# Performance work log

Measured on AMD Instinct MI355X. Metric: run time of the kernel, lower is better.

Reference implementation:

```python
import jax, jax.numpy as jnp
import numpy as np
import math

B, S, H = 2, 4096, 512
NUM_HEADS = 8
HEAD_DIM = H // NUM_HEADS
RECENCY_DECAY = 0.9


def setup_inputs() -> dict:
    key = jax.random.key(0)
    k1, k2, k3 = jax.random.split(key, 3)
    scale = 1.0 / math.sqrt(H)
    x = jax.random.normal(k1, (B, S, H), dtype=jnp.float32)
    w_qkv = jax.random.normal(k2, (3 * H, H), dtype=jnp.float32) * scale
    w_out = jax.random.normal(k3, (H, H), dtype=jnp.float32) * scale
    b_out = jnp.zeros((H,), dtype=jnp.float32)
    return {"x": x, "w_qkv": w_qkv, "w_out": w_out, "b_out": b_out}


def reference(x, w_qkv, w_out, b_out):
    batch, seq_len, hidden = x.shape
    nh, hd = NUM_HEADS, HEAD_DIM
    # qkv projection (no bias): torch Linear computes x @ W.T
    qkv = jnp.einsum('bsh,oh->bso', x, w_qkv)
    qkv = qkv.reshape(batch, seq_len, 3, nh, hd)
    q, k, v = jnp.transpose(qkv, (2, 0, 3, 1, 4))  # each [B, nh, S, hd]
    attn = jnp.einsum('bhqd,bhkd->bhqk', q, k) / math.sqrt(hd)
    # recency bias: positions[i, j] = j - i; bias = (j-i)*log(decay) for j<=i else 0
    pos = jnp.arange(seq_len)[None, :] - jnp.arange(seq_len)[:, None]
    bias = jnp.where(pos <= 0, pos.astype(jnp.float32) * math.log(RECENCY_DECAY),
                     jnp.zeros((), dtype=jnp.float32))
    attn = jax.nn.softmax(attn + bias[None, None, :, :], axis=-1)
    out = jnp.einsum('bhqk,bhkd->bqhd', attn, v).reshape(batch, seq_len, hidden)
    return jnp.einsum('bsh,oh->bso', out, w_out) + b_out
```

## Files before the change

kernel.cpp:

```cpp
#include <hip/hip_runtime.h>
#include <hip/hip_bf16.h>
#include <stdint.h>

#define B_   2
#define S_   4096
#define H_   512
#define NH_  8
#define HD_  64
#define M_   (B_*S_)
#define LOG2D (-0.15200309344504997f)
#define SC2   (0.18033688011112042f)

#define NFULL        6
#define NCHUNK       8

typedef __attribute__((ext_vector_type(8))) short bf16x8_t;
typedef __attribute__((ext_vector_type(4))) float f32x4_t;

__device__ __forceinline__ void gl_lds16(const __hip_bfloat16* g, __hip_bfloat16* l) {
  __builtin_amdgcn_global_load_lds(
      (__attribute__((address_space(1))) void*)(g),
      (__attribute__((address_space(3))) void*)(l),
      16, 0, 0);
}

__global__ __launch_bounds__(256)
void cast3_kernel(const float* __restrict__ x, const float* __restrict__ wq,
                  const float* __restrict__ wo,
                  __hip_bfloat16* __restrict__ xb, __hip_bfloat16* __restrict__ wqb,
                  __hip_bfloat16* __restrict__ wob) {
  const int N0 = M_ * H_;
  const int N1 = 3 * H_ * H_;
  int i4 = (blockIdx.x * blockDim.x + threadIdx.x) * 4;
  const float* src; __hip_bfloat16* dst; int off;
  if (i4 < N0)           { src = x;  dst = xb;  off = i4; }
  else if (i4 < N0 + N1) { src = wq; dst = wqb; off = i4 - N0; }
  else                   { src = wo; dst = wob; off = i4 - N0 - N1; }
  float4 v = *(const float4*)(src + off);
  ushort4 o;
  __hip_bfloat16 h;
  h = __float2bfloat16(v.x); o.x = *(unsigned short*)&h;
  h = __float2bfloat16(v.y); o.y = *(unsigned short*)&h;
  h = __float2bfloat16(v.z); o.z = *(unsigned short*)&h;
  h = __float2bfloat16(v.w); o.w = *(unsigned short*)&h;
  *(ushort4*)((unsigned short*)dst + off) = o;
}

template<int EPI>
__global__ __launch_bounds__(256)
void gemm_bt(const __hip_bfloat16* __restrict__ A,
             const __hip_bfloat16* __restrict__ Bw,
             int K,
             __hip_bfloat16* __restrict__ qb,
             __hip_bfloat16* __restrict__ kb,
             __hip_bfloat16* __restrict__ vtb,
             float* __restrict__ outp,
             const float* __restrict__ bias) {
  __shared__ alignas(16) __hip_bfloat16 sA[128*32];
  __shared__ alignas(16) __hip_bfloat16 sB[128*32];
  const int tid  = threadIdx.x;
  const int wave = tid >> 6, lane = tid & 63;
  const int quad = lane >> 4, l15 = lane & 15;
  const int wr = (wave >> 1) * 64, wc = (wave & 1) * 64;
  const int m0 = blockIdx.y * 128, n0 = blockIdx.x * 128;

  f32x4_t acc[4][4] = {};

  for (int kt = 0; kt < K; kt += 32) {
    __syncthreads();
    #pragma unroll
    for (int cc = 0; cc < 2; cc++) {
      int c   = wave * 2 + cc;
      int row = c * 16 + (lane >> 2);
      int col = (lane & 3) * 8;
      gl_lds16(A  + (size_t)(m0 + row) * K + kt + col, sA + c * 512);
      gl_lds16(Bw + (size_t)(n0 + row) * K + kt + col, sB + c * 512);
    }
    __syncthreads();
    bf16x8_t af[4], bfr[4];
    #pragma unroll
    for (int x = 0; x < 4; x++)
      af[x] = *(const bf16x8_t*)(sA + (wr + x*16 + l15)*32 + quad*8);
    #pragma unroll
    for (int y = 0; y < 4; y++)
      bfr[y] = *(const bf16x8_t*)(sB + (wc + y*16 + l15)*32 + quad*8);
    #pragma unroll
    for (int x = 0; x < 4; x++)
      #pragma unroll
      for (int y = 0; y < 4; y++)
        acc[x][y] = __builtin_amdgcn_mfma_f32_16x16x32_bf16(af[x], bfr[y], acc[x][y], 0, 0, 0);
  }

  #pragma unroll
  for (int x = 0; x < 4; x++) {
    #pragma unroll
    for (int y = 0; y < 4; y++) {
      #pragma unroll
      for (int r = 0; r < 4; r++) {
        int gr = m0 + wr + x*16 + quad*4 + r;
        int gc = n0 + wc + y*16 + l15;
        float v = acc[x][y][r];
        if (EPI == 0) {
          int bb = gr >> 12, s = gr & 4095;
          int t  = gc >> 9,  rem = gc & 511;
          int h  = rem >> 6, d = rem & 63;
          __hip_bfloat16 hv = __float2bfloat16(v);
          int bh = bb * NH_ + h;
          if (t == 0)      qb [((size_t)bh * S_ + s) * HD_ + d] = hv;
          else if (t == 1) kb [((size_t)bh * S_ + s) * HD_ + d] = hv;
          else             vtb[((size_t)bh * HD_ + d) * S_ + s] = hv;
        } else {
          outp[(size_t)gr * H_ + gc] = v + bias[gc];
        }
      }
    }
  }
}

__device__ __forceinline__ void stage_kv(const __hip_bfloat16* __restrict__ kb,
                                         const __hip_bfloat16* __restrict__ vtb,
                                         int bh, int j0,
                                         __hip_bfloat16* dK, __hip_bfloat16* dV,
                                         int wave, int lane) {
  const int subK  = lane >> 3;
  const int plogK = (lane & 7) ^ subK;
  const int subV  = lane >> 4;
  #pragma unroll
  for (int cc = 0; cc < 4; cc++) {
    int c = wave * 4 + cc;
    int rK = c * 8 + subK;
    gl_lds16(kb + ((size_t)bh * S_ + j0 + rK) * HD_ + plogK * 8, dK + c * 512);
    int rV = c * 4 + subV;
    int plogV = (lane & 15) ^ (rV & 15);
    gl_lds16(vtb + ((size_t)bh * HD_ + rV) * S_ + j0 + plogV * 8, dV + c * 512);
  }
}

__global__ __launch_bounds__(256)
void attn_kernel(const __hip_bfloat16* __restrict__ qb,
                 const __hip_bfloat16* __restrict__ kb,
                 const __hip_bfloat16* __restrict__ vtb,
                 __hip_bfloat16* __restrict__ ob,
                 float* __restrict__ pO,
                 float* __restrict__ pl) {
  __shared__ alignas(16) __hip_bfloat16 sK[2][128*64];
  __shared__ alignas(16) __hip_bfloat16 sV[2][64*128];
  __shared__ alignas(16) __hip_bfloat16 sP[4][16*128];

  const int tid  = threadIdx.x;
  const int wave = tid >> 6, lane = tid & 63;
  const int quad = lane >> 4, l15 = lane & 15;
  const int w  = blockIdx.x;
  const int bh = blockIdx.y;

  int qt, jt0;
  bool direct;
  if (w < 58) { qt = 6 + w;     jt0 = 0;            direct = true;  }
  else        { int t = w - 58; qt = t >> 3; jt0 = (t & 7) * 4; direct = false; }
  const int q0 = qt * 64;

  const int qr = q0 + wave * 16 + l15;
  const __hip_bfloat16* qrow = qb + ((size_t)bh * S_ + qr) * HD_;
  bf16x8_t aQ0 = *(const bf16x8_t*)(qrow + quad * 8);
  bf16x8_t aQ1 = *(const bf16x8_t*)(qrow + 32 + quad * 8);

  f32x4_t accO[4] = {};
  float l_r[4];
  float negM2[4];
  const int row_i = q0 + wave * 16 + quad * 4;
  #pragma unroll
  for (int r = 0; r < 4; r++) {
    l_r[r] = 0.f;
    negM2[r] = -(17.312340f - LOG2D * (float)(row_i + r));
  }

  stage_kv(kb, vtb, bh, jt0 * 128, &sK[0][0], &sV[0][0], wave, lane);

  for (int it = 0; it < 4; ++it) {
    const int j0 = (jt0 + it) * 128;
    __syncthreads();
    if (it < 3)
      stage_kv(kb, vtb, bh, (jt0 + it + 1) * 128,
               &sK[(it + 1) & 1][0], &sV[(it + 1) & 1][0], wave, lane);

    const __hip_bfloat16* cK = &sK[it & 1][0];
    const __hip_bfloat16* cV = &sV[it & 1][0];

    f32x4_t sfr[8];
    #pragma unroll
    for (int ni = 0; ni < 8; ni++) {
      int row = ni * 16 + l15;
      f32x4_t a = {};
      bf16x8_t b0 = *(const bf16x8_t*)(cK + row * 64 + ((quad       ^ (row & 7)) << 3));
      bf16x8_t b1 = *(const bf16x8_t*)(cK + row * 64 + (((quad + 4) ^ (row & 7)) << 3));
      a = __builtin_amdgcn_mfma_f32_16x16x32_bf16(aQ0, b0, a, 0, 0, 0);
      a = __builtin_amdgcn_mfma_f32_16x16x32_bf16(aQ1, b1, a, 0, 0, 0);
      sfr[ni] = a;
    }

    __hip_bfloat16* sPw = &sP[wave][0];
    const int mode = (j0 + 128 <= q0) ? 0 : ((j0 >= q0 + 64) ? 1 : 2);
    if (mode == 0) {
      float cj[8];
      #pragma unroll
      for (int ni = 0; ni < 8; ni++)
        cj[ni] = fmaf((float)(j0 + ni * 16 + l15), LOG2D, -17.312340f);
      #pragma unroll
      for (int r = 0; r < 4; r++) {
        const int row = quad * 4 + r;
        float psum = 0.f;
        #pragma unroll
        for (int ni = 0; ni < 8; ni++) {
          float p = __builtin_amdgcn_exp2f(fmaf(sfr[ni][r], SC2, cj[ni]));
          psum += p;
          int col = ni * 16 + l15;
          sPw[row * 128 + (((col >> 3) ^ (row & 15)) << 3) + (col & 7)] = __float2bfloat16(p);
        }
        l_r[r] += psum;
      }
    } else if (mode == 1) {
      #pragma unroll
      for (int r = 0; r < 4; r++) {
        const int row = quad * 4 + r;
        float psum = 0.f;
        #pragma unroll
        for (int ni = 0; ni < 8; ni++) {
          float p = __builtin_amdgcn_exp2f(fmaf(sfr[ni][r], SC2, negM2[r]));
          psum += p;
          int col = ni * 16 + l15;
          sPw[row * 128 + (((col >> 3) ^ (row & 15)) << 3) + (col & 7)] = __float2bfloat16(p);
        }
        l_r[r] += psum;
      }
    } else {
      #pragma unroll
      for (int r = 0; r < 4; r++) {
        const float d0 = (float)(j0 + l15 - (row_i + r));
        const int row = quad * 4 + r;
        float psum = 0.f;
        #pragma unroll
        for (int ni = 0; ni < 8; ni++) {
          float dij = d0 + (float)(ni * 16);
          float arg = fmaf(fminf(dij, 0.f), LOG2D, fmaf(sfr[ni][r], SC2, negM2[r]));
          float p = __builtin_amdgcn_exp2f(arg);
          psum += p;
          int col = ni * 16 + l15;
          sPw[row * 128 + (((col >> 3) ^ (row & 15)) << 3) + (col & 7)] = __float2bfloat16(p);
        }
        l_r[r] += psum;
      }
    }
    __builtin_amdgcn_sched_barrier(0);
    __builtin_amdgcn_s_waitcnt(0xC07F);
    __builtin_amdgcn_sched_barrier(0);

    #pragma unroll
    for (int kk = 0; kk < 4; kk++) {
      int pos = kk * 4 + quad;
      bf16x8_t aP = *(const bf16x8_t*)(sPw + l15 * 128 + ((pos ^ l15) << 3));
      #pragma unroll
      for (int nd = 0; nd < 4; nd++) {
        int row = nd * 16 + l15;
        bf16x8_t bV = *(const bf16x8_t*)(cV + row * 128 + ((pos ^ (row & 15)) << 3));
        accO[nd] = __builtin_amdgcn_mfma_f32_16x16x32_bf16(aP, bV, accO[nd], 0, 0, 0);
      }
    }
  }

  if (direct) {
    #pragma unroll
    for (int r = 0; r < 4; r++) {
      float l = l_r[r];
      #pragma unroll
      for (int msk = 1; msk < 16; msk <<= 1) l += __shfl_xor(l, msk, 64);
      l_r[r] = 1.0f / l;
    }
    const int b = bh >> 3, h = bh & 7;
    #pragma unroll
    for (int nd = 0; nd < 4; nd++)
      #pragma unroll
      for (int r = 0; r < 4; r++) {
        int srow = q0 + wave * 16 + quad * 4 + r;
        int col  = h * HD_ + nd * 16 + l15;
        ob[((size_t)b * S_ + srow) * H_ + col] = __float2bfloat16(accO[nd][r] * l_r[r]);
      }
  } else {
    #pragma unroll
    for (int r = 0; r < 4; r++) {
      float l = l_r[r];
      #pragma unroll
      for (int msk = 1; msk < 16; msk <<= 1) l += __shfl_xor(l, msk, 64);
      l_r[r] = l;
    }
    size_t base = ((size_t)bh * NFULL + qt) * NCHUNK + (size_t)(jt0 >> 2);
    float* po = pO + base * 4096;
    #pragma unroll
    for (int nd = 0; nd < 4; nd++)
      #pragma unroll
      for (int r = 0; r < 4; r++)
        po[(wave*16 + quad*4 + r) * 64 + nd*16 + l15] = accO[nd][r];
    if (l15 == 0) {
      #pragma unroll
      for (int r = 0; r < 4; r++)
        pl[base * 64 + wave*16 + quad*4 + r] = l_r[r];
    }
  }
}

__global__ __launch_bounds__(256)
void combine_kernel(const float* __restrict__ pO,
                    const float* __restrict__ pl,
                    __hip_bfloat16* __restrict__ ob) {
  const int f  = blockIdx.x;
  const int bh = blockIdx.y;
  const int tid = threadIdx.x;
  const int rr = tid >> 2, cg = (tid & 3) * 16;
  const size_t base0 = ((size_t)bh * NFULL + f) * NCHUNK;

  float L = 0.f;
  #pragma unroll
  for (int c = 0; c < NCHUNK; c++) L += pl[(base0 + c) * 64 + rr];
  const float inv = 1.0f / L;

  float o[16];
  #pragma unroll
  for (int k = 0; k < 16; k++) o[k] = 0.f;
  #pragma unroll
  for (int c = 0; c < NCHUNK; c++) {
    const float4* src = (const float4*)(pO + (base0 + c) * 4096 + rr * 64 + cg);
    #pragma unroll
    for (int k4 = 0; k4 < 4; k4++) {
      float4 v = src[k4];
      o[k4*4+0] += v.x; o[k4*4+1] += v.y;
      o[k4*4+2] += v.z; o[k4*4+3] += v.w;
    }
  }
  const int b = bh >> 3, h = bh & 7, s = f * 64 + rr;
  __hip_bfloat16* dst = ob + ((size_t)b * S_ + s) * H_ + h * HD_ + cg;
  #pragma unroll
  for (int k = 0; k < 16; k++) dst[k] = __float2bfloat16(o[k] * inv);
}

extern "C" void kernel_launch(void* const* d_in, const int* in_sizes, int n_in,
                              void* d_out, int out_size, void* d_ws, size_t ws_size,
                              hipStream_t stream) {
  const float* x     = (const float*)d_in[0];
  const float* w_qkv = (const float*)d_in[1];
  const float* w_out = (const float*)d_in[2];
  const float* b_out = (const float*)d_in[3];
  float* out = (float*)d_out;

  char* ws = (char*)d_ws;
  __hip_bfloat16* xb  = (__hip_bfloat16*)(ws);
  __hip_bfloat16* wqb = (__hip_bfloat16*)(ws + (8u  << 20));
  __hip_bfloat16* wob = (__hip_bfloat16*)(ws + (10u << 20));
  __hip_bfloat16* qb  = (__hip_bfloat16*)(ws + (11u << 20));
  __hip_bfloat16* kb  = (__hip_bfloat16*)(ws + (19u << 20));
  __hip_bfloat16* vtb = (__hip_bfloat16*)(ws + (27u << 20));
  float*          pO  = (float*)(ws + (36u << 20));
  float*          pl  = (float*)(ws + (49u << 20));
  __hip_bfloat16* ab  = xb;

  cast3_kernel<<<dim3(5120), dim3(256), 0, stream>>>(x, w_qkv, w_out, xb, wqb, wob);
  gemm_bt<0><<<dim3(12, 64), dim3(256), 0, stream>>>(xb, wqb, H_, qb, kb, vtb, nullptr, nullptr);
  attn_kernel<<<dim3(58 + NFULL * NCHUNK, B_ * NH_), dim3(256), 0, stream>>>(qb, kb, vtb, ab, pO, pl);
  combine_kernel<<<dim3(NFULL, B_ * NH_), dim3(256), 0, stream>>>(pO, pl, ab);
  gemm_bt<1><<<dim3(4, 64), dim3(256), 0, stream>>>(ab, wob, H_, nullptr, nullptr, nullptr, out, b_out);
}
```

Baseline: 162.3 us.

## Process 128 query rows per attention block and drop K/V double buffering

Each attention block now covers 128 query rows, two 16-row groups per wave, so every staged K/V tile is reused across twice as many queries. This halves the grid and the total K/V staging traffic. The double-buffered LDS prefetch is replaced by a single buffer with a load-then-sync per tile, which cuts LDS use but exposes global load latency. Split-K partial indexing is remapped so the combine kernel keeps its 64-row layout.

```diff
diff --git a/kernel.cpp b/kernel.cpp
--- a/kernel.cpp
+++ b/kernel.cpp
@@ -11,7 +11,6 @@
 #define LOG2D (-0.15200309344504997f)
 #define SC2   (0.18033688011112042f)
 
-#define NFULL        6
 #define NCHUNK       8
 
 typedef __attribute__((ext_vector_type(8))) short bf16x8_t;
@@ -143,8 +142,8 @@
                  __hip_bfloat16* __restrict__ ob,
                  float* __restrict__ pO,
                  float* __restrict__ pl) {
-  __shared__ alignas(16) __hip_bfloat16 sK[2][128*64];
-  __shared__ alignas(16) __hip_bfloat16 sV[2][64*128];
+  __shared__ alignas(16) __hip_bfloat16 sK[128*64];
+  __shared__ alignas(16) __hip_bfloat16 sV[64*128];
   __shared__ alignas(16) __hip_bfloat16 sP[4][16*128];
 
   const int tid  = threadIdx.x;
@@ -153,156 +152,169 @@
   const int w  = blockIdx.x;
   const int bh = blockIdx.y;
 
-  int qt, jt0;
+  int q0, jt0;
   bool direct;
-  if (w < 58) { qt = 6 + w;     jt0 = 0;            direct = true;  }
-  else        { int t = w - 58; qt = t >> 3; jt0 = (t & 7) * 4; direct = false; }
-  const int q0 = qt * 64;
-
-  const int qr = q0 + wave * 16 + l15;
-  const __hip_bfloat16* qrow = qb + ((size_t)bh * S_ + qr) * HD_;
-  bf16x8_t aQ0 = *(const bf16x8_t*)(qrow + quad * 8);
-  bf16x8_t aQ1 = *(const bf16x8_t*)(qrow + 32 + quad * 8);
-
-  f32x4_t accO[4] = {};
-  float l_r[4];
-  float negM2[4];
-  const int row_i = q0 + wave * 16 + quad * 4;
-  #pragma unroll
-  for (int r = 0; r < 4; r++) {
-    l_r[r] = 0.f;
-    negM2[r] = -(17.312340f - LOG2D * (float)(row_i + r));
-  }
-
-  stage_kv(kb, vtb, bh, jt0 * 128, &sK[0][0], &sV[0][0], wave, lane);
+  if (w < 29) { q0 = 384 + w * 128; jt0 = 0;           direct = true;  }
+  else { int t = w - 29; q0 = (t >> 3) * 128; jt0 = (t & 7) * 4; direct = false; }
+
+  const int rgb0 = q0 + wave * 32;
+  bf16x8_t aQ[2][2];
+  #pragma unroll
+  for (int g = 0; g < 2; g++) {
+    const __hip_bfloat16* qrow = qb + ((size_t)bh * S_ + rgb0 + g * 16 + l15) * HD_;
+    aQ[g][0] = *(const bf16x8_t*)(qrow + quad * 8);
+    aQ[g][1] = *(const bf16x8_t*)(qrow + 32 + quad * 8);
+  }
+
+  f32x4_t accO[2][4] = {};
+  float l_r[2][4];
+  float negM2[2][4];
+  #pragma unroll
+  for (int g = 0; g < 2; g++)
+    #pragma unroll
+    for (int r = 0; r < 4; r++) {
+      l_r[g][r] = 0.f;
+      negM2[g][r] = -(17.312340f - LOG2D * (float)(rgb0 + g * 16 + quad * 4 + r));
+    }
+
+  __hip_bfloat16* sPw = &sP[wave][0];
 
   for (int it = 0; it < 4; ++it) {
     const int j0 = (jt0 + it) * 128;
     __syncthreads();
-    if (it < 3)
-      stage_kv(kb, vtb, bh, (jt0 + it + 1) * 128,
-               &sK[(it + 1) & 1][0], &sV[(it + 1) & 1][0], wave, lane);
-
-    const __hip_bfloat16* cK = &sK[it & 1][0];
-    const __hip_bfloat16* cV = &sV[it & 1][0];
-
-    f32x4_t sfr[8];
-    #pragma unroll
-    for (int ni = 0; ni < 8; ni++) {
-      int row = ni * 16 + l15;
-      f32x4_t a = {};
-      bf16x8_t b0 = *(const bf16x8_t*)(cK + row * 64 + ((quad       ^ (row & 7)) << 3));
-      bf16x8_t b1 = *(const bf16x8_t*)(cK + row * 64 + (((quad + 4) ^ (row & 7)) << 3));
-      a = __builtin_amdgcn_mfma_f32_16x16x32_bf16(aQ0, b0, a, 0, 0, 0);
-      a = __builtin_amdgcn_mfma_f32_16x16x32_bf16(aQ1, b1, a, 0, 0, 0);
-      sfr[ni] = a;
-    }
-
-    __hip_bfloat16* sPw = &sP[wave][0];
-    const int mode = (j0 + 128 <= q0) ? 0 : ((j0 >= q0 + 64) ? 1 : 2);
-    if (mode == 0) {
-      float cj[8];
-      #pragma unroll
-      for (int ni = 0; ni < 8; ni++)
-        cj[ni] = fmaf((float)(j0 + ni * 16 + l15), LOG2D, -17.312340f);
+    stage_kv(kb, vtb, bh, j0, sK, sV, wave, lane);
+    __syncthreads();
+
+    #pragma unroll
+    for (int g = 0; g < 2; ++g) {
+      const int rgb = rgb0 + g * 16;
+
+      f32x4_t sfr[8];
+      #pragma unroll
+      for (int ni = 0; ni < 8; ni++) {
+        int row = ni * 16 + l15;
+        f32x4_t a = {};
+        bf16x8_t b0 = *(const bf16x8_t*)(sK + row * 64 + ((quad       ^ (row & 7)) << 3));
+        bf16x8_t b1 = *(const bf16x8_t*)(sK + row * 64 + (((quad + 4) ^ (row & 7)) << 3));
+        a = __builtin_amdgcn_mfma_f32_16x16x32_bf16(aQ[g][0], b0, a, 0, 0, 0);
+        a = __builtin_amdgcn_mfma_f32_16x16x32_bf16(aQ[g][1], b1, a, 0, 0, 0);
+        sfr[ni] = a;
+      }
+
+      const int mode = (j0 + 128 <= rgb) ? 0 : ((j0 >= rgb + 16) ? 1 : 2);
+      if (mode == 0) {
+        float cj[8];
+        #pragma unroll
+        for (int ni = 0; ni < 8; ni++)
+          cj[ni] = fmaf((float)(j0 + ni * 16 + l15), LOG2D, -17.312340f);
+        #pragma unroll
+        for (int r = 0; r < 4; r++) {
+          const int row = quad * 4 + r;
+          float psum = 0.f;
+          #pragma unroll
+          for (int ni = 0; ni < 8; ni++) {
+            float p = __builtin_amdgcn_exp2f(fmaf(sfr[ni][r], SC2, cj[ni]));
+            psum += p;
+            int col = ni * 16 + l15;
+            sPw[row * 128 + (((col >> 3) ^ (row & 15)) << 3) + (col & 7)] = __float2bfloat16(p);
+          }
+          l_r[g][r] += psum;
+        }
+      } else if (mode == 1) {
+        #pragma unroll
+        for (int r = 0; r < 4; r++) {
+          const int row = quad * 4 + r;
+          float psum = 0.f;
+          #pragma unroll
+          for (int ni = 0; ni < 8; ni++) {
+            float p = __builtin_amdgcn_exp2f(fmaf(sfr[ni][r], SC2, negM2[g][r]));
+            psum += p;
+            int col = ni * 16 + l15;
+            sPw[row * 128 + (((col >> 3) ^ (row & 15)) << 3) + (col & 7)] = __float2bfloat16(p);
+          }
+          l_r[g][r] += psum;
+        }
+      } else {
+        #pragma unroll
+        for (int r = 0; r < 4; r++) {
+          const float d0 = (float)(j0 + l15 - (rgb + quad * 4 + r));
+          const int row = quad * 4 + r;
+          float psum = 0.f;
+          #pragma unroll
+          for (int ni = 0; ni < 8; ni++) {
+            float dij = d0 + (float)(ni * 16);
+            float arg = fmaf(fminf(dij, 0.f), LOG2D, fmaf(sfr[ni][r], SC2, negM2[g][r]));
+            float p = __builtin_amdgcn_exp2f(arg);
+            psum += p;
+            int col = ni * 16 + l15;
+            sPw[row * 128 + (((col >> 3) ^ (row & 15)) << 3) + (col & 7)] = __float2bfloat16(p);
+          }
+          l_r[g][r] += psum;
+        }
+      }
+      __builtin_amdgcn_sched_barrier(0);
+      __builtin_amdgcn_s_waitcnt(0xC07F);
+      __builtin_amdgcn_sched_barrier(0);
+
+      #pragma unroll
+      for (int kk = 0; kk < 4; kk++) {
+        int pos = kk * 4 + quad;
+        bf16x8_t aP = *(const bf16x8_t*)(sPw + l15 * 128 + ((pos ^ l15) << 3));
+        #pragma unroll
+        for (int nd = 0; nd < 4; nd++) {
+          int row = nd * 16 + l15;
+          bf16x8_t bV = *(const bf16x8_t*)(sV + row * 128 + ((pos ^ (row & 15)) << 3));
+          accO[g][nd] = __builtin_amdgcn_mfma_f32_16x16x32_bf16(aP, bV, accO[g][nd], 0, 0, 0);
+        }
+      }
+      __builtin_amdgcn_sched_barrier(0);
+    }
+  }
+
+  if (direct) {
+    const int b = bh >> 3, h = bh & 7;
+    #pragma unroll
+    for (int g = 0; g < 2; g++) {
       #pragma unroll
       for (int r = 0; r < 4; r++) {
-        const int row = quad * 4 + r;
-        float psum = 0.f;
-        #pragma unroll
-        for (int ni = 0; ni < 8; ni++) {
-          float p = __builtin_amdgcn_exp2f(fmaf(sfr[ni][r], SC2, cj[ni]));
-          psum += p;
-          int col = ni * 16 + l15;
-          sPw[row * 128 + (((col >> 3) ^ (row & 15)) << 3) + (col & 7)] = __float2bfloat16(p);
-        }
-        l_r[r] += psum;
-      }
-    } else if (mode == 1) {
+        float l = l_r[g][r];
+        #pragma unroll
+        for (int msk = 1; msk < 16; msk <<= 1) l += __shfl_xor(l, msk, 64);
+        l_r[g][r] = 1.0f / l;
+      }
+      #pragma unroll
+      for (int nd = 0; nd < 4; nd++)
+        #pragma unroll
+        for (int r = 0; r < 4; r++) {
+          int srow = rgb0 + g * 16 + quad * 4 + r;
+          int col  = h * HD_ + nd * 16 + l15;
+          ob[((size_t)b * S_ + srow) * H_ + col] = __float2bfloat16(accO[g][nd][r] * l_r[g][r]);
+        }
+    }
+  } else {
+    const int qt   = (q0 >> 6) + (wave >> 1);
+    const int rbase = (wave & 1) * 32;
+    size_t base = ((size_t)bh * 6 + qt) * NCHUNK + (size_t)(jt0 >> 2);
+    float* po = pO + base * 4096;
+    #pragma unroll
+    for (int g = 0; g < 2; g++) {
       #pragma unroll
       for (int r = 0; r < 4; r++) {
-        const int row = quad * 4 + r;
-        float psum = 0.f;
-        #pragma unroll
-        for (int ni = 0; ni < 8; ni++) {
-          float p = __builtin_amdgcn_exp2f(fmaf(sfr[ni][r], SC2, negM2[r]));
-          psum += p;
-          int col = ni * 16 + l15;
-          sPw[row * 128 + (((col >> 3) ^ (row & 15)) << 3) + (col & 7)] = __float2bfloat16(p);
-        }
-        l_r[r] += psum;
-      }
-    } else {
-      #pragma unroll
-      for (int r = 0; r < 4; r++) {
-        const float d0 = (float)(j0 + l15 - (row_i + r));
-        const int row = quad * 4 + r;
-        float psum = 0.f;
-        #pragma unroll
-        for (int ni = 0; ni < 8; ni++) {
-          float dij = d0 + (float)(ni * 16);
-          float arg = fmaf(fminf(dij, 0.f), LOG2D, fmaf(sfr[ni][r], SC2, negM2[r]));
-          float p = __builtin_amdgcn_exp2f(arg);
-          psum += p;
-          int col = ni * 16 + l15;
-          sPw[row * 128 + (((col >> 3) ^ (row & 15)) << 3) + (col & 7)] = __float2bfloat16(p);
-        }
-        l_r[r] += psum;
-      }
-    }
-    __builtin_amdgcn_sched_barrier(0);
-    __builtin_amdgcn_s_waitcnt(0xC07F);
-    __builtin_amdgcn_sched_barrier(0);
-
-    #pragma unroll
-    for (int kk = 0; kk < 4; kk++) {
-      int pos = kk * 4 + quad;
-      bf16x8_t aP = *(const bf16x8_t*)(sPw + l15 * 128 + ((pos ^ l15) << 3));
-      #pragma unroll
-      for (int nd = 0; nd < 4; nd++) {
-        int row = nd * 16 + l15;
-        bf16x8_t bV = *(const bf16x8_t*)(cV + row * 128 + ((pos ^ (row & 15)) << 3));
-        accO[nd] = __builtin_amdgcn_mfma_f32_16x16x32_bf16(aP, bV, accO[nd], 0, 0, 0);
-      }
-    }
-  }
-
-  if (direct) {
-    #pragma unroll
-    for (int r = 0; r < 4; r++) {
-      float l = l_r[r];
-      #pragma unroll
-      for (int msk = 1; msk < 16; msk <<= 1) l += __shfl_xor(l, msk, 64);
-      l_r[r] = 1.0f / l;
-    }
-    const int b = bh >> 3, h = bh & 7;
-    #pragma unroll
-    for (int nd = 0; nd < 4; nd++)
-      #pragma unroll
-      for (int r = 0; r < 4; r++) {
-        int srow = q0 + wave * 16 + quad * 4 + r;
-        int col  = h * HD_ + nd * 16 + l15;
-        ob[((size_t)b * S_ + srow) * H_ + col] = __float2bfloat16(accO[nd][r] * l_r[r]);
-      }
-  } else {
-    #pragma unroll
-    for (int r = 0; r < 4; r++) {
-      float l = l_r[r];
-      #pragma unroll
-      for (int msk = 1; msk < 16; msk <<= 1) l += __shfl_xor(l, msk, 64);
-      l_r[r] = l;
-    }
-    size_t base = ((size_t)bh * NFULL + qt) * NCHUNK + (size_t)(jt0 >> 2);
-    float* po = pO + base * 4096;
-    #pragma unroll
-    for (int nd = 0; nd < 4; nd++)
-      #pragma unroll
-      for (int r = 0; r < 4; r++)
-        po[(wave*16 + quad*4 + r) * 64 + nd*16 + l15] = accO[nd][r];
-    if (l15 == 0) {
-      #pragma unroll
-      for (int r = 0; r < 4; r++)
-        pl[base * 64 + wave*16 + quad*4 + r] = l_r[r];
+        float l = l_r[g][r];
+        #pragma unroll
+        for (int msk = 1; msk < 16; msk <<= 1) l += __shfl_xor(l, msk, 64);
+        l_r[g][r] = l;
+      }
+      #pragma unroll
+      for (int nd = 0; nd < 4; nd++)
+        #pragma unroll
+        for (int r = 0; r < 4; r++)
+          po[(rbase + g*16 + quad*4 + r) * 64 + nd*16 + l15] = accO[g][nd][r];
+      if (l15 == 0) {
+        #pragma unroll
+        for (int r = 0; r < 4; r++)
+          pl[base * 64 + rbase + g*16 + quad*4 + r] = l_r[g][r];
+      }
     }
   }
 }
@@ -315,7 +327,7 @@
   const int bh = blockIdx.y;
   const int tid = threadIdx.x;
   const int rr = tid >> 2, cg = (tid & 3) * 16;
-  const size_t base0 = ((size_t)bh * NFULL + f) * NCHUNK;
+  const size_t base0 = ((size_t)bh * 6 + f) * NCHUNK;
 
   float L = 0.f;
   #pragma unroll
@@ -363,7 +375,7 @@
 
   cast3_kernel<<<dim3(5120), dim3(256), 0, stream>>>(x, w_qkv, w_out, xb, wqb, wob);
   gemm_bt<0><<<dim3(12, 64), dim3(256), 0, stream>>>(xb, wqb, H_, qb, kb, vtb, nullptr, nullptr);
-  attn_kernel<<<dim3(58 + NFULL * NCHUNK, B_ * NH_), dim3(256), 0, stream>>>(qb, kb, vtb, ab, pO, pl);
-  combine_kernel<<<dim3(NFULL, B_ * NH_), dim3(256), 0, stream>>>(pO, pl, ab);
+  attn_kernel<<<dim3(29 + 3 * NCHUNK, B_ * NH_), dim3(256), 0, stream>>>(qb, kb, vtb, ab, pO, pl);
+  combine_kernel<<<dim3(6, B_ * NH_), dim3(256), 0, stream>>>(pO, pl, ab);
   gemm_bt<1><<<dim3(4, 64), dim3(256), 0, stream>>>(ab, wob, H_, nullptr, nullptr, nullptr, out, b_out);
 }
```

Result: no change. 159.7 us (-1.6%).
